# Kernel tuning notes

Hardware: AMD Instinct MI355X
Metric: run time of the kernel (lower is better)

## Reference

```python
import jax, jax.numpy as jnp
import numpy as np

LENGTH_OF_SIGNAL = 2560
OUTLIER_THRESHOLD = 3.0


def setup_inputs() -> dict:
    key = jax.random.key(0)
    inputs = jax.random.normal(key, (16384, 2560, 1), dtype=jnp.float32)
    return {"inputs": inputs}


def reference(inputs):
    # inputs: (B, S, 1). All stats reduce over the sequence axis (dim=1).
    B, S, _ = inputs.shape
    x = inputs[..., 0]  # (B, S)

    mean = jnp.mean(x, axis=1)                       # (B,)
    maximum = jnp.max(x, axis=1)
    minimum = jnp.min(x, axis=1)
    p2p = maximum - minimum
    rms = jnp.sqrt(jnp.mean(x * x, axis=1))
    var = jnp.var(x, axis=1, ddof=1)                 # torch.var is unbiased
    std = jnp.sqrt(var)                              # torch.std is unbiased

    centered = x - mean[:, None]
    skewness = jnp.mean(centered ** 3, axis=1) / (std ** 3)
    kurtosis = jnp.mean(centered ** 4, axis=1) / (std ** 4)

    abs_x = jnp.abs(x)
    abs_sum = jnp.sum(abs_x, axis=1)
    abs_max = jnp.max(abs_x, axis=1)
    shape_factor = rms * LENGTH_OF_SIGNAL / abs_sum
    impulse_factor = abs_max * LENGTH_OF_SIGNAL / abs_sum

    outliers = jnp.sum(
        (jnp.abs(centered) > OUTLIER_THRESHOLD * std[:, None]).astype(jnp.int32),
        axis=1,
    ).astype(jnp.float32)

    # zero-crossing rate on flattened (B, S) signal
    zcr = jnp.sum(
        (jnp.diff(jnp.sign(x), axis=1) != 0).astype(jnp.float32), axis=1
    ) / (2.0 * S)

    # Hjorth parameters (activity, mobility, complexity)
    d1 = jnp.diff(x, axis=1)
    d2 = jnp.diff(d1, axis=1)
    var_d1 = jnp.var(d1, axis=1, ddof=1)
    var_d2 = jnp.var(d2, axis=1, ddof=1)
    activity = var
    mobility = jnp.sqrt(var_d1 / var)
    complexity = jnp.sqrt(var_d2 / var_d1)

    stacked = jnp.stack(
        [mean, maximum, minimum, p2p, var, rms, skewness, kurtosis,
         shape_factor, impulse_factor, outliers, zcr,
         activity, mobility, complexity],
        axis=1,
    )  # (B, 15)
    return stacked
```

## Files before the change

### kernel.cpp

```cpp
#include <hip/hip_runtime.h>
#include <math.h>


constexpr int S_LEN = 2560;

__global__ __launch_bounds__(256)
void health_stats_kernel(const float* __restrict__ in, float* __restrict__ out) {
    const int lane = threadIdx.x & 63;
    const int wave = threadIdx.x >> 6;
    const int row  = blockIdx.x * 4 + wave;

    const float* rp = in + (size_t)row * S_LEN + lane * 4;

    float xr[40];
    double sum = 0.0, sq = 0.0;
    float sabs = 0.0f, vmax = -INFINITY, vmin = INFINITY;

#pragma unroll
    for (int k = 0; k < 10; k += 2) {
        float4 a = *reinterpret_cast<const float4*>(rp + k * 256);
        float4 b = *reinterpret_cast<const float4*>(rp + (k + 1) * 256);
        xr[4*k+0]=a.x; xr[4*k+1]=a.y; xr[4*k+2]=a.z; xr[4*k+3]=a.w;
        xr[4*k+4]=b.x; xr[4*k+5]=b.y; xr[4*k+6]=b.z; xr[4*k+7]=b.w;

        float s8 = ((a.x + a.y) + (a.z + a.w)) + ((b.x + b.y) + (b.z + b.w));
        float q8 = fmaf(a.x, a.x, fmaf(a.y, a.y, fmaf(a.z, a.z, a.w * a.w)))
                 + fmaf(b.x, b.x, fmaf(b.y, b.y, fmaf(b.z, b.z, b.w * b.w)));
        sum += (double)s8;
        sq  += (double)q8;

        sabs += ((fabsf(a.x) + fabsf(a.y)) + (fabsf(a.z) + fabsf(a.w)))
              + ((fabsf(b.x) + fabsf(b.y)) + (fabsf(b.z) + fabsf(b.w)));
        vmax = fmaxf(vmax, fmaxf(fmaxf(fmaxf(a.x, a.y), fmaxf(a.z, a.w)),
                                 fmaxf(fmaxf(b.x, b.y), fmaxf(b.z, b.w))));
        vmin = fminf(vmin, fminf(fminf(fminf(a.x, a.y), fminf(a.z, a.w)),
                                 fminf(fminf(b.x, b.y), fminf(b.z, b.w))));
    }

#pragma unroll
    for (int o = 32; o > 0; o >>= 1) {
        sum  += __shfl_xor(sum, o);
        sq   += __shfl_xor(sq, o);
        sabs += __shfl_xor(sabs, o);
        vmax  = fmaxf(vmax, __shfl_xor(vmax, o));
        vmin  = fminf(vmin, __shfl_xor(vmin, o));
    }

    const double mean = sum * (1.0 / S_LEN);
    const double var  = (sq - sum * mean) * (1.0 / (S_LEN - 1));
    const double stdv = sqrt(var);
    const double thr  = 3.0 * stdv;

    const double bhi = mean + thr, blo = mean - thr;
    float bhi_f = (float)bhi;
    if ((double)bhi_f > bhi) bhi_f = __int_as_float(__float_as_int(bhi_f) - 1);
    float blo_f = (float)blo;
    if ((double)blo_f < blo) blo_f = __int_as_float(__float_as_int(blo_f) - 1);

    const float mf = (float)mean;
    float c3s = 0.f, c4s = 0.f, s1q = 0.f, s2q = 0.f;
    int outc = 0, zcc = 0;

#pragma unroll
    for (int k = 0; k < 10; ++k) {
        const float x0 = xr[4*k+0], x1 = xr[4*k+1], x2v = xr[4*k+2], x3 = xr[4*k+3];
        const int kn = (k == 9) ? 0 : (k + 1);
        float v0 = (lane == 0) ? xr[4*kn+0] : x0;
        float v1 = (lane == 0) ? xr[4*kn+1] : x1;
        const float n0 = __shfl(v0, (lane + 1) & 63);
        const float n1 = __shfl(v1, (lane + 1) & 63);

        const float c0 = x0 - mf, c1 = x1 - mf, c2 = x2v - mf, c3 = x3 - mf;
        const float q0 = c0*c0, q1 = c1*c1, q2 = c2*c2, q3 = c3*c3;
        c3s = fmaf(q0, c0, fmaf(q1, c1, fmaf(q2, c2, fmaf(q3, c3, c3s))));
        c4s = fmaf(q0, q0, fmaf(q1, q1, fmaf(q2, q2, fmaf(q3, q3, c4s))));

        outc += __popcll(__ballot(x0  > bhi_f || x0  < blo_f));
        outc += __popcll(__ballot(x1  > bhi_f || x1  < blo_f));
        outc += __popcll(__ballot(x2v > bhi_f || x2v < blo_f));
        outc += __popcll(__ballot(x3  > bhi_f || x3  < blo_f));

        const float d10 = x1 - x0, d11 = x2v - x1, d12 = x3 - x2v;
        const float d13 = n0 - x3,  d14 = n1 - n0;
        const float e0 = d11 - d10, e1 = d12 - d11, e2 = d13 - d12, e3 = d14 - d13;

        const int b0 = __float_as_int(x0), b1 = __float_as_int(x1),
                  b2 = __float_as_int(x2v), b3 = __float_as_int(x3),
                  bn = __float_as_int(n0);

        if (k < 9) {
            s1q = fmaf(d10, d10, fmaf(d11, d11, fmaf(d12, d12, fmaf(d13, d13, s1q))));
            s2q = fmaf(e0, e0, fmaf(e1, e1, fmaf(e2, e2, fmaf(e3, e3, s2q))));
            zcc += __popcll(__ballot((b0 ^ b1) < 0));
            zcc += __popcll(__ballot((b1 ^ b2) < 0));
            zcc += __popcll(__ballot((b2 ^ b3) < 0));
            zcc += __popcll(__ballot((b3 ^ bn) < 0));
        } else {
            const bool ok = lane < 63;
            s1q = fmaf(d10, d10, fmaf(d11, d11, fmaf(d12, d12, s1q)));
            s1q += ok ? d13 * d13 : 0.f;
            s2q = fmaf(e0, e0, fmaf(e1, e1, s2q));
            s2q += ok ? e2 * e2 : 0.f;
            s2q += ok ? e3 * e3 : 0.f;
            zcc += __popcll(__ballot((b0 ^ b1) < 0));
            zcc += __popcll(__ballot((b1 ^ b2) < 0));
            zcc += __popcll(__ballot((b2 ^ b3) < 0));
            zcc += __popcll(__ballot(((b3 ^ bn) < 0) && ok));
        }
    }

#pragma unroll
    for (int o = 32; o > 0; o >>= 1) {
        c3s += __shfl_xor(c3s, o);
        c4s += __shfl_xor(c4s, o);
        s1q += __shfl_xor(s1q, o);
        s2q += __shfl_xor(s2q, o);
    }

    const float e0f = __shfl(xr[0], 0);
    const float e1f = __shfl(xr[1], 0);
    const float f2f = __shfl(xr[38], 63);
    const float f3f = __shfl(xr[39], 63);

    if (lane == 0) {
        const double rms  = sqrt(sq * (1.0 / S_LEN));
        const double m3   = (double)c3s * (1.0 / S_LEN);
        const double m4   = (double)c4s * (1.0 / S_LEN);
        const double skew = m3 / (var * stdv);
        const double kurt = m4 / (var * var);
        const float  amax = fmaxf(fabsf(vmax), fabsf(vmin));
        const double shape   = rms * (double)S_LEN / (double)sabs;
        const double impulse = (double)amax * (double)S_LEN / (double)sabs;
        const double s1 = (double)f3f - (double)e0f;
        const double s2 = ((double)f3f - (double)f2f) - ((double)e1f - (double)e0f);
        const double var1 = ((double)s1q - s1 * s1 * (1.0 / (S_LEN - 1))) * (1.0 / (S_LEN - 2));
        const double var2 = ((double)s2q - s2 * s2 * (1.0 / (S_LEN - 2))) * (1.0 / (S_LEN - 3));

        float* o = out + (size_t)row * 15;
        o[0]  = (float)mean;
        o[1]  = vmax;
        o[2]  = vmin;
        o[3]  = vmax - vmin;
        o[4]  = (float)var;
        o[5]  = (float)rms;
        o[6]  = (float)skew;
        o[7]  = (float)kurt;
        o[8]  = (float)shape;
        o[9]  = (float)impulse;
        o[10] = (float)outc;
        o[11] = (float)zcc * (1.0f / (2.0f * S_LEN));
        o[12] = (float)var;
        o[13] = (float)sqrt(var1 / var);
        o[14] = (float)sqrt(var2 / var1);
    }
}

extern "C" void kernel_launch(void* const* d_in, const int* in_sizes, int n_in,
                              void* d_out, int out_size, void* d_ws, size_t ws_size,
                              hipStream_t stream) {
    (void)in_sizes; (void)n_in; (void)d_ws; (void)ws_size; (void)out_size;
    const float* in = (const float*)d_in[0];
    float* out = (float*)d_out;
    health_stats_kernel<<<4096, 256, 0, stream>>>(in, out);
}
```

Before: 42.23 us.

## Split each row across two waves and combine partial statistics via LDS

Each row is now processed by two waves, each covering half the samples. Partial sums, extrema, boundary samples and higher-moment partials are exchanged through shared memory with block barriers. This halves per-thread register arrays and doubles the grid, aiming for higher occupancy and more loads in flight. The cost is two block-wide synchronisations and extra LDS traffic per row.

```diff
diff --git a/kernel.cpp b/kernel.cpp
--- a/kernel.cpp
+++ b/kernel.cpp
@@ -3,38 +3,49 @@
 
 
 constexpr int S_LEN = 2560;
+constexpr int HALF  = 1280;
+
+struct RowLds {
+    double sum[2];
+    double sq[2];
+    float  sabs[2], vmax[2], vmin[2];
+    float  nb0, nb1;
+    float  ep0, ep1, ep2, ep3;
+    float  c3s[2], c4s[2], s1q[2], s2q[2];
+    float  outc[2], zcc[2];
+};
 
 __global__ __launch_bounds__(256)
 void health_stats_kernel(const float* __restrict__ in, float* __restrict__ out) {
+    __shared__ RowLds lds[2];
+
     const int lane = threadIdx.x & 63;
-    const int wave = threadIdx.x >> 6;
-    const int row  = blockIdx.x * 4 + wave;
-
-    const float* rp = in + (size_t)row * S_LEN + lane * 4;
-
-    float xr[40];
+    const int wid  = threadIdx.x >> 6;
+    const int hidx = wid & 1;
+    const int rsl  = wid >> 1;
+    const int row  = blockIdx.x * 2 + rsl;
+
+    RowLds& L = lds[rsl];
+
+    const float* rp = in + (size_t)row * S_LEN + hidx * HALF + lane * 4;
+
+    float xr[20];
+    float s8a = 0.f, q8a = 0.f;
     double sum = 0.0, sq = 0.0;
-    float sabs = 0.0f, vmax = -INFINITY, vmin = INFINITY;
-
-#pragma unroll
-    for (int k = 0; k < 10; k += 2) {
+    float sabs = 0.f, vmax = -INFINITY, vmin = INFINITY;
+
+#pragma unroll
+    for (int k = 0; k < 5; ++k) {
         float4 a = *reinterpret_cast<const float4*>(rp + k * 256);
-        float4 b = *reinterpret_cast<const float4*>(rp + (k + 1) * 256);
         xr[4*k+0]=a.x; xr[4*k+1]=a.y; xr[4*k+2]=a.z; xr[4*k+3]=a.w;
-        xr[4*k+4]=b.x; xr[4*k+5]=b.y; xr[4*k+6]=b.z; xr[4*k+7]=b.w;
-
-        float s8 = ((a.x + a.y) + (a.z + a.w)) + ((b.x + b.y) + (b.z + b.w));
-        float q8 = fmaf(a.x, a.x, fmaf(a.y, a.y, fmaf(a.z, a.z, a.w * a.w)))
-                 + fmaf(b.x, b.x, fmaf(b.y, b.y, fmaf(b.z, b.z, b.w * b.w)));
-        sum += (double)s8;
-        sq  += (double)q8;
-
-        sabs += ((fabsf(a.x) + fabsf(a.y)) + (fabsf(a.z) + fabsf(a.w)))
-              + ((fabsf(b.x) + fabsf(b.y)) + (fabsf(b.z) + fabsf(b.w)));
-        vmax = fmaxf(vmax, fmaxf(fmaxf(fmaxf(a.x, a.y), fmaxf(a.z, a.w)),
-                                 fmaxf(fmaxf(b.x, b.y), fmaxf(b.z, b.w))));
-        vmin = fminf(vmin, fminf(fminf(fminf(a.x, a.y), fminf(a.z, a.w)),
-                                 fminf(fminf(b.x, b.y), fminf(b.z, b.w))));
+        float s4 = (a.x + a.y) + (a.z + a.w);
+        float q4 = fmaf(a.x,a.x, fmaf(a.y,a.y, fmaf(a.z,a.z, a.w*a.w)));
+        if ((k & 1) == 0) { s8a = s4; q8a = q4; }
+        else              { sum += (double)(s8a + s4); sq += (double)(q8a + q4); }
+        if (k == 4)       { sum += (double)s4; sq += (double)q4; }
+        sabs += (fabsf(a.x)+fabsf(a.y)) + (fabsf(a.z)+fabsf(a.w));
+        vmax = fmaxf(vmax, fmaxf(fmaxf(a.x,a.y), fmaxf(a.z,a.w)));
+        vmin = fminf(vmin, fminf(fminf(a.x,a.y), fminf(a.z,a.w)));
     }
 
 #pragma unroll
@@ -46,8 +57,20 @@
         vmin  = fminf(vmin, __shfl_xor(vmin, o));
     }
 
-    const double mean = sum * (1.0 / S_LEN);
-    const double var  = (sq - sum * mean) * (1.0 / (S_LEN - 1));
+    if (lane == 0) {
+        L.sum[hidx] = sum;  L.sq[hidx] = sq;
+        L.sabs[hidx] = sabs; L.vmax[hidx] = vmax; L.vmin[hidx] = vmin;
+        if (hidx == 0) { L.ep0 = xr[0]; L.ep1 = xr[1]; }
+        else           { L.nb0 = xr[0]; L.nb1 = xr[1]; }
+    }
+    if (lane == 63 && hidx == 1) { L.ep2 = xr[18]; L.ep3 = xr[19]; }
+
+    __syncthreads();
+
+    const double tsum = L.sum[0] + L.sum[1];
+    const double tsq  = L.sq[0]  + L.sq[1];
+    const double mean = tsum * (1.0 / S_LEN);
+    const double var  = (tsq - tsum * mean) * (1.0 / (S_LEN - 1));
     const double stdv = sqrt(var);
     const double thr  = 3.0 * stdv;
 
@@ -57,18 +80,21 @@
     float blo_f = (float)blo;
     if ((double)blo_f < blo) blo_f = __int_as_float(__float_as_int(blo_f) - 1);
 
+    const float nbv0 = L.nb0, nbv1 = L.nb1;
     const float mf = (float)mean;
+
     float c3s = 0.f, c4s = 0.f, s1q = 0.f, s2q = 0.f;
     int outc = 0, zcc = 0;
 
 #pragma unroll
-    for (int k = 0; k < 10; ++k) {
+    for (int k = 0; k < 5; ++k) {
         const float x0 = xr[4*k+0], x1 = xr[4*k+1], x2v = xr[4*k+2], x3 = xr[4*k+3];
-        const int kn = (k == 9) ? 0 : (k + 1);
+        const int kn = (k == 4) ? 0 : (k + 1);
         float v0 = (lane == 0) ? xr[4*kn+0] : x0;
         float v1 = (lane == 0) ? xr[4*kn+1] : x1;
-        const float n0 = __shfl(v0, (lane + 1) & 63);
-        const float n1 = __shfl(v1, (lane + 1) & 63);
+        float n0 = __shfl(v0, (lane + 1) & 63);
+        float n1 = __shfl(v1, (lane + 1) & 63);
+        if (k == 4 && lane == 63) { n0 = nbv0; n1 = nbv1; }
 
         const float c0 = x0 - mf, c1 = x1 - mf, c2 = x2v - mf, c3 = x3 - mf;
         const float q0 = c0*c0, q1 = c1*c1, q2 = c2*c2, q3 = c3*c3;
@@ -81,30 +107,27 @@
         outc += __popcll(__ballot(x3  > bhi_f || x3  < blo_f));
 
         const float d10 = x1 - x0, d11 = x2v - x1, d12 = x3 - x2v;
-        const float d13 = n0 - x3,  d14 = n1 - n0;
+        const float d13 = n0 - x3, d14 = n1 - n0;
         const float e0 = d11 - d10, e1 = d12 - d11, e2 = d13 - d12, e3 = d14 - d13;
 
         const int b0 = __float_as_int(x0), b1 = __float_as_int(x1),
                   b2 = __float_as_int(x2v), b3 = __float_as_int(x3),
                   bn = __float_as_int(n0);
-
-        if (k < 9) {
+        zcc += __popcll(__ballot((b0 ^ b1) < 0));
+        zcc += __popcll(__ballot((b1 ^ b2) < 0));
+        zcc += __popcll(__ballot((b2 ^ b3) < 0));
+
+        if (k < 4) {
             s1q = fmaf(d10, d10, fmaf(d11, d11, fmaf(d12, d12, fmaf(d13, d13, s1q))));
             s2q = fmaf(e0, e0, fmaf(e1, e1, fmaf(e2, e2, fmaf(e3, e3, s2q))));
-            zcc += __popcll(__ballot((b0 ^ b1) < 0));
-            zcc += __popcll(__ballot((b1 ^ b2) < 0));
-            zcc += __popcll(__ballot((b2 ^ b3) < 0));
             zcc += __popcll(__ballot((b3 ^ bn) < 0));
         } else {
-            const bool ok = lane < 63;
+            const bool ok = (hidx == 0) || (lane < 63);
             s1q = fmaf(d10, d10, fmaf(d11, d11, fmaf(d12, d12, s1q)));
             s1q += ok ? d13 * d13 : 0.f;
             s2q = fmaf(e0, e0, fmaf(e1, e1, s2q));
             s2q += ok ? e2 * e2 : 0.f;
             s2q += ok ? e3 * e3 : 0.f;
-            zcc += __popcll(__ballot((b0 ^ b1) < 0));
-            zcc += __popcll(__ballot((b1 ^ b2) < 0));
-            zcc += __popcll(__ballot((b2 ^ b3) < 0));
             zcc += __popcll(__ballot(((b3 ^ bn) < 0) && ok));
         }
     }
@@ -117,38 +140,51 @@
         s2q += __shfl_xor(s2q, o);
     }
 
-    const float e0f = __shfl(xr[0], 0);
-    const float e1f = __shfl(xr[1], 0);
-    const float f2f = __shfl(xr[38], 63);
-    const float f3f = __shfl(xr[39], 63);
-
     if (lane == 0) {
-        const double rms  = sqrt(sq * (1.0 / S_LEN));
-        const double m3   = (double)c3s * (1.0 / S_LEN);
-        const double m4   = (double)c4s * (1.0 / S_LEN);
+        L.c3s[hidx] = c3s;  L.c4s[hidx] = c4s;
+        L.s1q[hidx] = s1q;  L.s2q[hidx] = s2q;
+        L.outc[hidx] = (float)outc;  L.zcc[hidx] = (float)zcc;
+    }
+
+    __syncthreads();
+
+    if (hidx == 0 && lane == 0) {
+        const float tabs = L.sabs[0] + L.sabs[1];
+        const float tmax = fmaxf(L.vmax[0], L.vmax[1]);
+        const float tmin = fminf(L.vmin[0], L.vmin[1]);
+        const float c3t  = L.c3s[0] + L.c3s[1];
+        const float c4t  = L.c4s[0] + L.c4s[1];
+        const float s1qt = L.s1q[0] + L.s1q[1];
+        const float s2qt = L.s2q[0] + L.s2q[1];
+        const float outt = L.outc[0] + L.outc[1];
+        const float zct  = L.zcc[0] + L.zcc[1];
+
+        const double rms  = sqrt(tsq * (1.0 / S_LEN));
+        const double m3   = (double)c3t * (1.0 / S_LEN);
+        const double m4   = (double)c4t * (1.0 / S_LEN);
         const double skew = m3 / (var * stdv);
         const double kurt = m4 / (var * var);
-        const float  amax = fmaxf(fabsf(vmax), fabsf(vmin));
-        const double shape   = rms * (double)S_LEN / (double)sabs;
-        const double impulse = (double)amax * (double)S_LEN / (double)sabs;
-        const double s1 = (double)f3f - (double)e0f;
-        const double s2 = ((double)f3f - (double)f2f) - ((double)e1f - (double)e0f);
-        const double var1 = ((double)s1q - s1 * s1 * (1.0 / (S_LEN - 1))) * (1.0 / (S_LEN - 2));
-        const double var2 = ((double)s2q - s2 * s2 * (1.0 / (S_LEN - 2))) * (1.0 / (S_LEN - 3));
+        const float  amax = fmaxf(fabsf(tmax), fabsf(tmin));
+        const double shape   = rms * (double)S_LEN / (double)tabs;
+        const double impulse = (double)amax * (double)S_LEN / (double)tabs;
+        const double s1 = (double)L.ep3 - (double)L.ep0;
+        const double s2 = ((double)L.ep3 - (double)L.ep2) - ((double)L.ep1 - (double)L.ep0);
+        const double var1 = ((double)s1qt - s1 * s1 * (1.0 / (S_LEN - 1))) * (1.0 / (S_LEN - 2));
+        const double var2 = ((double)s2qt - s2 * s2 * (1.0 / (S_LEN - 2))) * (1.0 / (S_LEN - 3));
 
         float* o = out + (size_t)row * 15;
         o[0]  = (float)mean;
-        o[1]  = vmax;
-        o[2]  = vmin;
-        o[3]  = vmax - vmin;
+        o[1]  = tmax;
+        o[2]  = tmin;
+        o[3]  = tmax - tmin;
         o[4]  = (float)var;
         o[5]  = (float)rms;
         o[6]  = (float)skew;
         o[7]  = (float)kurt;
         o[8]  = (float)shape;
         o[9]  = (float)impulse;
-        o[10] = (float)outc;
-        o[11] = (float)zcc * (1.0f / (2.0f * S_LEN));
+        o[10] = outt;
+        o[11] = zct * (1.0f / (2.0f * S_LEN));
         o[12] = (float)var;
         o[13] = (float)sqrt(var1 / var);
         o[14] = (float)sqrt(var2 / var1);
@@ -161,5 +197,5 @@
     (void)in_sizes; (void)n_in; (void)d_ws; (void)ws_size; (void)out_size;
     const float* in = (const float*)d_in[0];
     float* out = (float*)d_out;
-    health_stats_kernel<<<4096, 256, 0, stream>>>(in, out);
+    health_stats_kernel<<<8192, 256, 0, stream>>>(in, out);
 }
```

After: 42.10 us. Within noise of the previous version (-0.3%).
